# Optimization experiments

Hardware: AMD Instinct MI355X
Metric: run time of the kernel (lower is better)

## Reference

```python
import jax, jax.numpy as jnp
import numpy as np

N, T, H = 4000, 32, 64      # N = batch_size*n_neurons, t_repetition, gcn_d
E = 1024000
NT = N * T                   # graph nodes after temporal unrolling
N_NEURONS = 500
B = N // N_NEURONS
T_EBD = 16                   # tau * t_repetition = 0.5*32
N_STEPS = 12


def setup_inputs() -> dict:
    key = jax.random.key(0)
    ks = jax.random.split(key, 13)
    s = 1.0 / np.sqrt(H)
    return {
        "node_features": jax.random.normal(ks[0], (N, T, H), jnp.float32),
        "edge_index_batch": jax.random.randint(ks[1], (2, E), 0, NT, jnp.int32),
        "edge_attr_batch": jax.random.uniform(ks[2], (E,), jnp.float32),
        "batch": jax.random.randint(ks[3], (N,), 0, B, jnp.int32),
        # GRU params (1 layer, torch layout: W_ih [3H,H], W_hh [3H,H])
        "gru_Wih": jax.random.normal(ks[4], (3 * H, H), jnp.float32) * s,
        "gru_Whh": jax.random.normal(ks[5], (3 * H, H), jnp.float32) * s,
        "gru_bih": jax.random.normal(ks[6], (3 * H,), jnp.float32) * s,
        "gru_bhh": jax.random.normal(ks[7], (3 * H,), jnp.float32) * s,
        # GCNConv linear weight [out,in], no bias
        "gcn_W": jax.random.normal(ks[8], (H, H), jnp.float32) * s,
        # temporal attention MLP: Linear(T->T_ebd), Linear(T_ebd->T), no bias
        "attn_W1": jax.random.normal(ks[9], (T_EBD, T), jnp.float32) * (1.0 / np.sqrt(T)),
        "attn_W2": jax.random.normal(ks[10], (T, T_EBD), jnp.float32) * (1.0 / np.sqrt(T_EBD)),
        # final head Linear(gcn_d -> n_steps) with bias
        "fc_W": jax.random.normal(ks[11], (N_STEPS, H), jnp.float32) * s,
        "fc_b": jax.random.normal(ks[12], (N_STEPS,), jnp.float32) * s,
    }


def _gru(x, Wih, Whh, bih, bhh):
    # x: [N, T, H] -> outputs [N, T, H] (torch GRU equations, h0 = 0)
    xg = x @ Wih.T + bih  # [N, T, 3H], input projection precomputed

    def step(h, xg_t):
        hg = h @ Whh.T + bhh
        xr, xz, xn = jnp.split(xg_t, 3, axis=-1)
        hr, hz, hn = jnp.split(hg, 3, axis=-1)
        r = jax.nn.sigmoid(xr + hr)
        z = jax.nn.sigmoid(xz + hz)
        n = jnp.tanh(xn + r * hn)
        h_new = (1.0 - z) * n + z * h
        return h_new, h_new

    h0 = jnp.zeros((x.shape[0], Whh.shape[1]), x.dtype)
    _, hs = jax.lax.scan(step, h0, jnp.swapaxes(xg, 0, 1))  # hs: [T, N, H]
    return jnp.swapaxes(hs, 0, 1)


def _gcn(x, W, edge_index, edge_weight, n_nodes):
    # PyG GCNConv: add self-loops (weight 1), symmetric deg^-1/2 norm, no bias
    loops = jnp.arange(n_nodes, dtype=edge_index.dtype)
    src = jnp.concatenate([edge_index[0], loops])
    dst = jnp.concatenate([edge_index[1], loops])
    w = jnp.concatenate([edge_weight, jnp.ones((n_nodes,), edge_weight.dtype)])
    xw = x @ W.T                                            # [NT, H]
    deg = jax.ops.segment_sum(w, dst, num_segments=n_nodes)
    dis = jnp.where(deg > 0, jax.lax.rsqrt(jnp.where(deg > 0, deg, 1.0)), 0.0)
    norm = dis[src] * w * dis[dst]                          # [E+NT]
    msgs = norm[:, None] * xw[src]                          # gather + scale
    return jax.ops.segment_sum(msgs, dst, num_segments=n_nodes)


def reference(node_features, edge_index_batch, edge_attr_batch, batch,
              gru_Wih, gru_Whh, gru_bih, gru_bhh, gcn_W,
              attn_W1, attn_W2, fc_W, fc_b):
    # DGRLayer: GRU over time, then GCN over the flattened (node,time) graph
    g = _gru(node_features, gru_Wih, gru_Whh, gru_bih, gru_bhh)  # [N, T, H]
    x = g.reshape(NT, H)
    x = _gcn(x, gcn_W, edge_index_batch, edge_attr_batch, NT)
    x3 = x.reshape(N, T, H)

    # TemporalAttention (reshape mirrors torch contiguous .view semantics)
    xt = x3.reshape(B, T, N_NEURONS * H).mean(axis=-1)           # [B, T]
    attn = jax.nn.sigmoid(jax.nn.relu(xt @ attn_W1.T) @ attn_W2.T)  # [B, T]

    nf = x3.reshape(B, T, N_NEURONS, H)
    pooled = jnp.sum(attn[:, :, None, None] * nf, axis=(1, 2))   # [B, H]
    return pooled @ fc_W.T + fc_b                                # [B, n_steps]
```

## Files before the change

kernel.cpp:

```cpp
#include <hip/hip_runtime.h>
#include <hip/hip_fp16.h>

#define NNODES   4000
#define TSTEPS   32
#define HDIM     64
#define ECOUNT   1024000
#define NTOT     128000
#define BATCHB   8
#define NNEUR    500
#define TEBD     16
#define NSTEPS   12

#define CNT_SHIFT 23
#define SUM_MASK  0x7FFFFFu
#define SUM_SCALE 262144.0f
#define SLOTS     32
#define REC_BLOCKS  (NNODES / 16)
#define HIST_BLOCKS (ECOUNT / 256)
#define SCALE_BLOCKS (NTOT * HDIM / 8 / 256)

#define ROWS_PER_WAVE  5
#define ROWS_PER_BLOCK 20
#define GATHER_BLOCKS  (NTOT / ROWS_PER_BLOCK)

typedef _Float16 half8_t __attribute__((ext_vector_type(8)));
typedef float    f32x4_t __attribute__((ext_vector_type(4)));

__device__ __forceinline__ float sigmoidf_(float x) {
    return 1.0f / (1.0f + __expf(-x));
}
__device__ __forceinline__ float tanhf_(float x) {
    return 1.0f - 2.0f / (1.0f + __expf(2.0f * x));
}

__global__ __launch_bounds__(256) void k_recHist(
    const float* __restrict__ x, const float* __restrict__ Wih,
    const float* __restrict__ Whh, const float* __restrict__ bih,
    const float* __restrict__ bhh, const float* __restrict__ Wg,
    _Float16* __restrict__ xwh,
    const int* __restrict__ ei, const float* __restrict__ ea,
    unsigned* __restrict__ dc, unsigned* __restrict__ se32)
{
    __shared__ __align__(16) _Float16 hbuf[2][16 * 72];

    const int tid = threadIdx.x;

    if (blockIdx.x >= REC_BLOCKS) {
        int e = (blockIdx.x - REC_BLOCKS) * 256 + tid;
        int s = ei[e], d = ei[ECOUNT + e];
        float w = ea[e];
        unsigned q = (unsigned)(w * 32768.0f + 0.5f); q = q > 32767u ? 32767u : q;
        unsigned fx = (unsigned)(w * SUM_SCALE + 0.5f);
        unsigned old = atomicAdd(&dc[d], (1u << CNT_SHIFT) | fx);
        int r = (int)(old >> CNT_SHIFT);
        if (r < SLOTS)
            se32[d * SLOTS + r] = ((unsigned)s << 15) | q;
        return;
    }

    const int lane = tid & 63;
    const int wv   = tid >> 6;
    const int c    = lane & 15;
    const int quad = lane >> 4;
    const int n0   = blockIdx.x * 16;

    auto makeB = [&](const float* W, int row, int k0) -> half8_t {
        const float4* p = (const float4*)(W + (size_t)row * HDIM + k0);
        float4 u = p[0], v = p[1];
        half8_t h;
        h[0] = (_Float16)u.x; h[1] = (_Float16)u.y; h[2] = (_Float16)u.z; h[3] = (_Float16)u.w;
        h[4] = (_Float16)v.x; h[5] = (_Float16)v.y; h[6] = (_Float16)v.z; h[7] = (_Float16)v.w;
        return h;
    };

    half8_t Bxr[2], Bxz[2], Bxn[2], Bhr[2], Bhz[2], Bhn[2], Bw[2];
#pragma unroll
    for (int kt = 0; kt < 2; ++kt) {
        int k0 = kt * 32 + quad * 8;
        Bxr[kt] = makeB(Wih, wv * 16 + c, k0);
        Bxz[kt] = makeB(Wih, 64 + wv * 16 + c, k0);
        Bxn[kt] = makeB(Wih, 128 + wv * 16 + c, k0);
        Bhr[kt] = makeB(Whh, wv * 16 + c, k0);
        Bhz[kt] = makeB(Whh, 64 + wv * 16 + c, k0);
        Bhn[kt] = makeB(Whh, 128 + wv * 16 + c, k0);
        Bw[kt]  = makeB(Wg, wv * 16 + c, k0);
    }

    const int f = wv * 16 + c;
    const float brz_r = bih[f] + bhh[f];
    const float brz_z = bih[64 + f] + bhh[64 + f];
    const float bin_  = bih[128 + f];
    const float bhn_  = bhh[128 + f];

    float hreg[4] = {0.f, 0.f, 0.f, 0.f};
    half8_t ah[2];

    const float* xp = x + (size_t)(n0 + c) * (TSTEPS * HDIM) + quad * 8;

    float4 xq0[4], xq1[4];
    {
        const float* p0 = xp;
        xq0[0] = *(const float4*)(p0);      xq0[1] = *(const float4*)(p0 + 4);
        xq0[2] = *(const float4*)(p0 + 32); xq0[3] = *(const float4*)(p0 + 36);
        const float* p1 = xp + HDIM;
        xq1[0] = *(const float4*)(p1);      xq1[1] = *(const float4*)(p1 + 4);
        xq1[2] = *(const float4*)(p1 + 32); xq1[3] = *(const float4*)(p1 + 36);
    }

    auto step = [&](int t, float4* xq) {
        half8_t ax[2];
#pragma unroll
        for (int kt = 0; kt < 2; ++kt) {
            float4 u = xq[kt * 2], v = xq[kt * 2 + 1];
            half8_t a;
            a[0] = (_Float16)u.x; a[1] = (_Float16)u.y; a[2] = (_Float16)u.z; a[3] = (_Float16)u.w;
            a[4] = (_Float16)v.x; a[5] = (_Float16)v.y; a[6] = (_Float16)v.z; a[7] = (_Float16)v.w;
            ax[kt] = a;
        }
        if (t + 2 < TSTEPS) {
            const float* pt = xp + (size_t)(t + 2) * HDIM;
            xq[0] = *(const float4*)(pt);      xq[1] = *(const float4*)(pt + 4);
            xq[2] = *(const float4*)(pt + 32); xq[3] = *(const float4*)(pt + 36);
        }

        f32x4_t Cr  = (f32x4_t){0.f, 0.f, 0.f, 0.f};
        f32x4_t Cz  = (f32x4_t){0.f, 0.f, 0.f, 0.f};
        f32x4_t Cnx = (f32x4_t){0.f, 0.f, 0.f, 0.f};
        f32x4_t Cnh = (f32x4_t){0.f, 0.f, 0.f, 0.f};

#pragma unroll
        for (int kt = 0; kt < 2; ++kt) {
            Cr  = __builtin_amdgcn_mfma_f32_16x16x32_f16(ax[kt], Bxr[kt], Cr, 0, 0, 0);
            Cz  = __builtin_amdgcn_mfma_f32_16x16x32_f16(ax[kt], Bxz[kt], Cz, 0, 0, 0);
            Cnx = __builtin_amdgcn_mfma_f32_16x16x32_f16(ax[kt], Bxn[kt], Cnx, 0, 0, 0);
        }
        if (t > 0) {
#pragma unroll
            for (int kt = 0; kt < 2; ++kt) {
                Cr  = __builtin_amdgcn_mfma_f32_16x16x32_f16(ah[kt], Bhr[kt], Cr, 0, 0, 0);
                Cz  = __builtin_amdgcn_mfma_f32_16x16x32_f16(ah[kt], Bhz[kt], Cz, 0, 0, 0);
                Cnh = __builtin_amdgcn_mfma_f32_16x16x32_f16(ah[kt], Bhn[kt], Cnh, 0, 0, 0);
            }
        }

        _Float16* hb = hbuf[t & 1];
#pragma unroll
        for (int r = 0; r < 4; ++r) {
            float rr = sigmoidf_(Cr[r] + brz_r);
            float zz = sigmoidf_(Cz[r] + brz_z);
            float nn = tanhf_(Cnx[r] + bin_ + rr * (Cnh[r] + bhn_));
            float hn = (1.0f - zz) * nn + zz * hreg[r];
            hreg[r] = hn;
            hb[(quad * 4 + r) * 72 + f] = (_Float16)hn;
        }

        __syncthreads();

#pragma unroll
        for (int kt = 0; kt < 2; ++kt)
            ah[kt] = *(half8_t*)&hb[c * 72 + kt * 32 + quad * 8];

        f32x4_t Cw = (f32x4_t){0.f, 0.f, 0.f, 0.f};
#pragma unroll
        for (int kt = 0; kt < 2; ++kt)
            Cw = __builtin_amdgcn_mfma_f32_16x16x32_f16(ah[kt], Bw[kt], Cw, 0, 0, 0);

#pragma unroll
        for (int r = 0; r < 4; ++r) {
            int row = (n0 + quad * 4 + r) * TSTEPS + t;
            xwh[(size_t)row * HDIM + f] = (_Float16)Cw[r];
        }
    };

#pragma unroll 1
    for (int tt = 0; tt < TSTEPS; tt += 2) {
        step(tt, xq0);
        step(tt + 1, xq1);
    }
}

__global__ __launch_bounds__(256) void k_scale(
    _Float16* __restrict__ xwh, const unsigned* __restrict__ dc)
{
    const int t = blockIdx.x * 256 + threadIdx.x;
    const int row = t >> 3;
    const float dd = rsqrtf(1.0f + (float)(dc[row] & SUM_MASK) * 0x1p-18f);
    half8_t v = *(half8_t*)&xwh[(size_t)t * 8];
#pragma unroll
    for (int i = 0; i < 8; ++i) v[i] = (_Float16)((float)v[i] * dd);
    *(half8_t*)&xwh[(size_t)t * 8] = v;
}

__global__ __launch_bounds__(256) void k_gather(
    const _Float16* __restrict__ xws, const unsigned* __restrict__ dc,
    const unsigned* __restrict__ se32, float* __restrict__ S)
{
    const int tid  = threadIdx.x;
    const int lane = tid & 63;
    const int wv   = tid >> 6;
    const int d0   = blockIdx.x * ROWS_PER_BLOCK + wv * ROWS_PER_WAVE;

    unsigned pk[ROWS_PER_WAVE];
    float    sf[ROWS_PER_WAVE];
#pragma unroll
    for (int i = 0; i < ROWS_PER_WAVE; ++i) pk[i] = dc[d0 + i];
#pragma unroll
    for (int i = 0; i < ROWS_PER_WAVE; ++i)
        sf[i] = (float)xws[(size_t)(d0 + i) * HDIM + lane];

    float acc = 0.f;
#pragma unroll
    for (int i = 0; i < ROWS_PER_WAVE; ++i) {
        const int d = d0 + i;
        const float dd = rsqrtf(1.0f + (float)(pk[i] & SUM_MASK) * 0x1p-18f);
        int cnt = (int)(pk[i] >> CNT_SHIFT);
        cnt = cnt < SLOTS ? cnt : SLOTS;
        const unsigned* bkt = se32 + (size_t)d * SLOTS;

        float a0 = sf[i];
        float a1 = 0.f, a2 = 0.f, a3 = 0.f;
        int j = 0;
        for (; j + 8 <= cnt; j += 8) {
            uint4 qa = *(const uint4*)(bkt + j);
            uint4 qb = *(const uint4*)(bkt + j + 4);
            float v0 = (float)xws[(size_t)(qa.x >> 15) * HDIM + lane];
            float v1 = (float)xws[(size_t)(qa.y >> 15) * HDIM + lane];
            float v2 = (float)xws[(size_t)(qa.z >> 15) * HDIM + lane];
            float v3 = (float)xws[(size_t)(qa.w >> 15) * HDIM + lane];
            float v4 = (float)xws[(size_t)(qb.x >> 15) * HDIM + lane];
            float v5 = (float)xws[(size_t)(qb.y >> 15) * HDIM + lane];
            float v6 = (float)xws[(size_t)(qb.z >> 15) * HDIM + lane];
            float v7 = (float)xws[(size_t)(qb.w >> 15) * HDIM + lane];
            a0 = fmaf((float)(qa.x & 0x7FFFu) * 0x1p-15f, v0, a0);
            a1 = fmaf((float)(qa.y & 0x7FFFu) * 0x1p-15f, v1, a1);
            a2 = fmaf((float)(qa.z & 0x7FFFu) * 0x1p-15f, v2, a2);
            a3 = fmaf((float)(qa.w & 0x7FFFu) * 0x1p-15f, v3, a3);
            a0 = fmaf((float)(qb.x & 0x7FFFu) * 0x1p-15f, v4, a0);
            a1 = fmaf((float)(qb.y & 0x7FFFu) * 0x1p-15f, v5, a1);
            a2 = fmaf((float)(qb.z & 0x7FFFu) * 0x1p-15f, v6, a2);
            a3 = fmaf((float)(qb.w & 0x7FFFu) * 0x1p-15f, v7, a3);
        }
        for (; j + 4 <= cnt; j += 4) {
            uint4 q = *(const uint4*)(bkt + j);
            float v0 = (float)xws[(size_t)(q.x >> 15) * HDIM + lane];
            float v1 = (float)xws[(size_t)(q.y >> 15) * HDIM + lane];
            float v2 = (float)xws[(size_t)(q.z >> 15) * HDIM + lane];
            float v3 = (float)xws[(size_t)(q.w >> 15) * HDIM + lane];
            a0 = fmaf((float)(q.x & 0x7FFFu) * 0x1p-15f, v0, a0);
            a1 = fmaf((float)(q.y & 0x7FFFu) * 0x1p-15f, v1, a1);
            a2 = fmaf((float)(q.z & 0x7FFFu) * 0x1p-15f, v2, a2);
            a3 = fmaf((float)(q.w & 0x7FFFu) * 0x1p-15f, v3, a3);
        }
        for (; j < cnt; ++j) {
            unsigned u = bkt[j];
            a0 = fmaf((float)(u & 0x7FFFu) * 0x1p-15f,
                      (float)xws[(size_t)(u >> 15) * HDIM + lane], a0);
        }
        acc = fmaf(dd, (a0 + a1) + (a2 + a3), acc);
    }

    __shared__ float red[256];
    red[tid] = acc;
    __syncthreads();
    if (tid < 64) {
        float s = red[tid] + red[64 + tid] + red[128 + tid] + red[192 + tid];
        atomicAdd(&S[((blockIdx.x * ROWS_PER_BLOCK) / NNEUR) * HDIM + tid], s);
    }
}

__global__ __launch_bounds__(256) void k_final(
    const float* __restrict__ S, const float* __restrict__ W1,
    const float* __restrict__ W2, const float* __restrict__ fcW,
    const float* __restrict__ fcb, float* __restrict__ out)
{
    __shared__ float xt[256];
    __shared__ float a1[128];
    __shared__ float attn[256];
    __shared__ float pooled[512];
    const int tid = threadIdx.x;

    {
        float s = 0.f;
        const float* p = S + tid * 64;
#pragma unroll
        for (int hh = 0; hh < 64; ++hh) s += p[hh];
        xt[tid] = s * (1.0f / 32000.0f);
    }
    __syncthreads();
    if (tid < 128) {
        int b = tid >> 4, i = tid & 15;
        float s = 0.f;
#pragma unroll
        for (int t = 0; t < 32; ++t) s += xt[b * 32 + t] * W1[i * 32 + t];
        a1[tid] = fmaxf(s, 0.f);
    }
    __syncthreads();
    {
        int b = tid >> 5, t = tid & 31;
        float s = 0.f;
#pragma unroll
        for (int i = 0; i < 16; ++i) s += a1[b * 16 + i] * W2[t * 16 + i];
        attn[tid] = 1.0f / (1.0f + __expf(-s));
    }
    __syncthreads();
    for (int o = tid; o < 512; o += 256) {
        int b = o >> 6, h = o & 63;
        float s = 0.f;
#pragma unroll
        for (int t = 0; t < 32; ++t) s += attn[b * 32 + t] * S[(b * 32 + t) * 64 + h];
        pooled[o] = s;
    }
    __syncthreads();
    if (tid < BATCHB * NSTEPS) {
        int b = tid / NSTEPS, st = tid % NSTEPS;
        float acc = fcb[st];
#pragma unroll
        for (int h = 0; h < 64; ++h) acc += pooled[b * 64 + h] * fcW[st * 64 + h];
        out[b * NSTEPS + st] = acc;
    }
}

extern "C" void kernel_launch(void* const* d_in, const int* in_sizes, int n_in,
                              void* d_out, int out_size, void* d_ws, size_t ws_size,
                              hipStream_t stream) {
    const float* x   = (const float*)d_in[0];
    const int*   ei  = (const int*)  d_in[1];
    const float* ea  = (const float*)d_in[2];
    const float* Wih = (const float*)d_in[4];
    const float* Whh = (const float*)d_in[5];
    const float* bih = (const float*)d_in[6];
    const float* bhh = (const float*)d_in[7];
    const float* Wg  = (const float*)d_in[8];
    const float* W1  = (const float*)d_in[9];
    const float* W2  = (const float*)d_in[10];
    const float* fcW = (const float*)d_in[11];
    const float* fcb = (const float*)d_in[12];
    float* out = (float*)d_out;

    char* p = (char*)d_ws;
    unsigned* dc = (unsigned*)p;   p += sizeof(unsigned) * NTOT;
    float* S = (float*)p;          p += sizeof(float) * 256 * HDIM;
    unsigned* se32 = (unsigned*)p; p += sizeof(unsigned) * (size_t)NTOT * SLOTS;
    _Float16* xwh = (_Float16*)p;  p += sizeof(_Float16) * (size_t)NTOT * HDIM;

    hipMemsetAsync(dc, 0, sizeof(unsigned) * NTOT + sizeof(float) * 256 * HDIM, stream);
    k_recHist <<<REC_BLOCKS + HIST_BLOCKS, 256, 0, stream>>>(
        x, Wih, Whh, bih, bhh, Wg, xwh, ei, ea, dc, se32);
    k_scale   <<<SCALE_BLOCKS, 256, 0, stream>>>(xwh, dc);
    k_gather  <<<GATHER_BLOCKS, 256, 0, stream>>>(xwh, dc, se32, S);
    k_final   <<<1, 256, 0, stream>>>(S, W1, W2, fcW, fcb, out);
}
```

Before: 228.9 us.

## Replace per-destination edge gather with dense source-by-group aggregation matrix GEMM

Only per-(batch,time) group sums of the GCN output are needed downstream. The change therefore accumulates normalized edge weights into a dense 16-bit fixed-point matrix indexed by source node and destination group, then multiplies it against the scaled features in a blocked fp16 multiply-accumulate kernel. Partial results are merged per group, together with self-loops. This removes the slot-based per-destination gather of feature rows, at the cost of zeroing and streaming a large matrix of about 65 MB. It also brings fixed-point packed atomics and fp16 accumulation that may lose precision or overflow. The old path is kept as a fallback when the workspace is too small.

```diff
diff --git a/kernel.cpp b/kernel.cpp
--- a/kernel.cpp
+++ b/kernel.cpp
@@ -11,19 +11,30 @@
 #define TEBD     16
 #define NSTEPS   12
 
+#define REC_BLOCKS  (NNODES / 16)
+
+#define HISTF_BLOCKS (ECOUNT / 256)
+#define ZERO_BLOCKS  2000
+#define NBT          256
+#define MBYTES       ((size_t)NTOT * NBT * 2)
+#define MB_BLOCKS    (ECOUNT / 256)
+#define SCALE_BLOCKS (NTOT * HDIM / 8 / 256)
+#define GEMM_BLOCKS  256
+#define CHUNK_SRC    (NTOT / GEMM_BLOCKS)
+#define PPART        (NBT * HDIM)
+#define MAIN_WS      (512000 + 65536 + 65536000 + 16777216 + 16384000)
+
 #define CNT_SHIFT 23
 #define SUM_MASK  0x7FFFFFu
 #define SUM_SCALE 262144.0f
 #define SLOTS     32
-#define REC_BLOCKS  (NNODES / 16)
 #define HIST_BLOCKS (ECOUNT / 256)
-#define SCALE_BLOCKS (NTOT * HDIM / 8 / 256)
-
 #define ROWS_PER_WAVE  5
 #define ROWS_PER_BLOCK 20
 #define GATHER_BLOCKS  (NTOT / ROWS_PER_BLOCK)
 
 typedef _Float16 half8_t __attribute__((ext_vector_type(8)));
+typedef _Float16 half2_t __attribute__((ext_vector_type(2)));
 typedef float    f32x4_t __attribute__((ext_vector_type(4)));
 
 __device__ __forceinline__ float sigmoidf_(float x) {
@@ -31,6 +42,253 @@
 }
 __device__ __forceinline__ float tanhf_(float x) {
     return 1.0f - 2.0f / (1.0f + __expf(2.0f * x));
+}
+
+__device__ __forceinline__ void gru_body(
+    const float* __restrict__ x, const float* __restrict__ Wih,
+    const float* __restrict__ Whh, const float* __restrict__ bih,
+    const float* __restrict__ bhh, const float* __restrict__ Wg,
+    _Float16* __restrict__ xwh, _Float16 (*hbuf)[16 * 72], int tid, int blk)
+{
+    const int lane = tid & 63;
+    const int wv   = tid >> 6;
+    const int c    = lane & 15;
+    const int quad = lane >> 4;
+    const int n0   = blk * 16;
+
+    auto makeB = [&](const float* W, int row, int k0) -> half8_t {
+        const float4* p = (const float4*)(W + (size_t)row * HDIM + k0);
+        float4 u = p[0], v = p[1];
+        half8_t h;
+        h[0] = (_Float16)u.x; h[1] = (_Float16)u.y; h[2] = (_Float16)u.z; h[3] = (_Float16)u.w;
+        h[4] = (_Float16)v.x; h[5] = (_Float16)v.y; h[6] = (_Float16)v.z; h[7] = (_Float16)v.w;
+        return h;
+    };
+
+    half8_t Bxr[2], Bxz[2], Bxn[2], Bhr[2], Bhz[2], Bhn[2], Bw[2];
+#pragma unroll
+    for (int kt = 0; kt < 2; ++kt) {
+        int k0 = kt * 32 + quad * 8;
+        Bxr[kt] = makeB(Wih, wv * 16 + c, k0);
+        Bxz[kt] = makeB(Wih, 64 + wv * 16 + c, k0);
+        Bxn[kt] = makeB(Wih, 128 + wv * 16 + c, k0);
+        Bhr[kt] = makeB(Whh, wv * 16 + c, k0);
+        Bhz[kt] = makeB(Whh, 64 + wv * 16 + c, k0);
+        Bhn[kt] = makeB(Whh, 128 + wv * 16 + c, k0);
+        Bw[kt]  = makeB(Wg, wv * 16 + c, k0);
+    }
+
+    const int f = wv * 16 + c;
+    const float brz_r = bih[f] + bhh[f];
+    const float brz_z = bih[64 + f] + bhh[64 + f];
+    const float bin_  = bih[128 + f];
+    const float bhn_  = bhh[128 + f];
+
+    float hreg[4] = {0.f, 0.f, 0.f, 0.f};
+    half8_t ah[2];
+
+    const float* xp = x + (size_t)(n0 + c) * (TSTEPS * HDIM) + quad * 8;
+
+    float4 xq0[4], xq1[4];
+    {
+        const float* p0 = xp;
+        xq0[0] = *(const float4*)(p0);      xq0[1] = *(const float4*)(p0 + 4);
+        xq0[2] = *(const float4*)(p0 + 32); xq0[3] = *(const float4*)(p0 + 36);
+        const float* p1 = xp + HDIM;
+        xq1[0] = *(const float4*)(p1);      xq1[1] = *(const float4*)(p1 + 4);
+        xq1[2] = *(const float4*)(p1 + 32); xq1[3] = *(const float4*)(p1 + 36);
+    }
+
+    auto step = [&](int t, float4* xq) {
+        half8_t ax[2];
+#pragma unroll
+        for (int kt = 0; kt < 2; ++kt) {
+            float4 u = xq[kt * 2], v = xq[kt * 2 + 1];
+            half8_t a;
+            a[0] = (_Float16)u.x; a[1] = (_Float16)u.y; a[2] = (_Float16)u.z; a[3] = (_Float16)u.w;
+            a[4] = (_Float16)v.x; a[5] = (_Float16)v.y; a[6] = (_Float16)v.z; a[7] = (_Float16)v.w;
+            ax[kt] = a;
+        }
+        if (t + 2 < TSTEPS) {
+            const float* pt = xp + (size_t)(t + 2) * HDIM;
+            xq[0] = *(const float4*)(pt);      xq[1] = *(const float4*)(pt + 4);
+            xq[2] = *(const float4*)(pt + 32); xq[3] = *(const float4*)(pt + 36);
+        }
+
+        f32x4_t Cr  = (f32x4_t){0.f, 0.f, 0.f, 0.f};
+        f32x4_t Cz  = (f32x4_t){0.f, 0.f, 0.f, 0.f};
+        f32x4_t Cnx = (f32x4_t){0.f, 0.f, 0.f, 0.f};
+        f32x4_t Cnh = (f32x4_t){0.f, 0.f, 0.f, 0.f};
+
+#pragma unroll
+        for (int kt = 0; kt < 2; ++kt) {
+            Cr  = __builtin_amdgcn_mfma_f32_16x16x32_f16(ax[kt], Bxr[kt], Cr, 0, 0, 0);
+            Cz  = __builtin_amdgcn_mfma_f32_16x16x32_f16(ax[kt], Bxz[kt], Cz, 0, 0, 0);
+            Cnx = __builtin_amdgcn_mfma_f32_16x16x32_f16(ax[kt], Bxn[kt], Cnx, 0, 0, 0);
+        }
+        if (t > 0) {
+#pragma unroll
+            for (int kt = 0; kt < 2; ++kt) {
+                Cr  = __builtin_amdgcn_mfma_f32_16x16x32_f16(ah[kt], Bhr[kt], Cr, 0, 0, 0);
+                Cz  = __builtin_amdgcn_mfma_f32_16x16x32_f16(ah[kt], Bhz[kt], Cz, 0, 0, 0);
+                Cnh = __builtin_amdgcn_mfma_f32_16x16x32_f16(ah[kt], Bhn[kt], Cnh, 0, 0, 0);
+            }
+        }
+
+        _Float16* hb = hbuf[t & 1];
+#pragma unroll
+        for (int r = 0; r < 4; ++r) {
+            float rr = sigmoidf_(Cr[r] + brz_r);
+            float zz = sigmoidf_(Cz[r] + brz_z);
+            float nn = tanhf_(Cnx[r] + bin_ + rr * (Cnh[r] + bhn_));
+            float hn = (1.0f - zz) * nn + zz * hreg[r];
+            hreg[r] = hn;
+            hb[(quad * 4 + r) * 72 + f] = (_Float16)hn;
+        }
+
+        __syncthreads();
+
+#pragma unroll
+        for (int kt = 0; kt < 2; ++kt)
+            ah[kt] = *(half8_t*)&hb[c * 72 + kt * 32 + quad * 8];
+
+        f32x4_t Cw = (f32x4_t){0.f, 0.f, 0.f, 0.f};
+#pragma unroll
+        for (int kt = 0; kt < 2; ++kt)
+            Cw = __builtin_amdgcn_mfma_f32_16x16x32_f16(ah[kt], Bw[kt], Cw, 0, 0, 0);
+
+#pragma unroll
+        for (int r = 0; r < 4; ++r) {
+            int row = (n0 + quad * 4 + r) * TSTEPS + t;
+            xwh[(size_t)row * HDIM + f] = (_Float16)Cw[r];
+        }
+    };
+
+#pragma unroll 1
+    for (int tt = 0; tt < TSTEPS; tt += 2) {
+        step(tt, xq0);
+        step(tt + 1, xq1);
+    }
+}
+
+
+__global__ __launch_bounds__(256) void k_recHZ(
+    const float* __restrict__ x, const float* __restrict__ Wih,
+    const float* __restrict__ Whh, const float* __restrict__ bih,
+    const float* __restrict__ bhh, const float* __restrict__ Wg,
+    _Float16* __restrict__ xwh,
+    const int* __restrict__ ei, const float* __restrict__ ea,
+    float* __restrict__ dw, uint4* __restrict__ Mz)
+{
+    __shared__ __align__(16) _Float16 hbuf[2][16 * 72];
+    const int tid = threadIdx.x;
+
+    if (blockIdx.x >= REC_BLOCKS + HISTF_BLOCKS) {
+        const int zb = blockIdx.x - (REC_BLOCKS + HISTF_BLOCKS);
+        uint4* p = Mz + (size_t)zb * 2048;
+        uint4 z; z.x = 0; z.y = 0; z.z = 0; z.w = 0;
+#pragma unroll
+        for (int i = 0; i < 8; ++i) p[i * 256 + tid] = z;
+        return;
+    }
+    if (blockIdx.x >= REC_BLOCKS) {
+        int e = (blockIdx.x - REC_BLOCKS) * 256 + tid;
+        atomicAdd(&dw[ei[ECOUNT + e]], ea[e]);
+        return;
+    }
+    gru_body(x, Wih, Whh, bih, bhh, Wg, xwh, hbuf, tid, blockIdx.x);
+}
+
+__global__ __launch_bounds__(256) void k_scaleF(
+    _Float16* __restrict__ xwh, const float* __restrict__ dw)
+{
+    const int t = blockIdx.x * 256 + threadIdx.x;
+    const int row = t >> 3;
+    const float dd = rsqrtf(1.0f + dw[row]);
+    half8_t v = *(half8_t*)&xwh[(size_t)t * 8];
+#pragma unroll
+    for (int i = 0; i < 8; ++i) v[i] = (_Float16)((float)v[i] * dd);
+    *(half8_t*)&xwh[(size_t)t * 8] = v;
+}
+
+__global__ __launch_bounds__(256) void k_Mbuild(
+    const int* __restrict__ ei, const float* __restrict__ ea,
+    const float* __restrict__ dw, unsigned* __restrict__ M32)
+{
+    int e = blockIdx.x * 256 + threadIdx.x;
+    int s = ei[e], d = ei[ECOUNT + e];
+    float c = ea[e] * rsqrtf(1.0f + dw[d]);
+    unsigned bt = (unsigned)d / 500u;
+    unsigned fx = (unsigned)(c * 4096.0f + 0.5f);
+    unsigned val = (bt & 1u) ? (fx << 16) : fx;
+    atomicAdd(&M32[(size_t)s * 128 + (bt >> 1)], val);
+}
+
+__global__ __launch_bounds__(512) void k_gemm(
+    const _Float16* __restrict__ xws, const unsigned short* __restrict__ Mu,
+    float* __restrict__ Ppart)
+{
+    const int tid = threadIdx.x;
+    const int bt  = tid & 255;
+    const int hh  = tid >> 8;
+    const int base = blockIdx.x * CHUNK_SRC;
+
+    half2_t acc2[16];
+#pragma unroll
+    for (int j = 0; j < 16; ++j) acc2[j] = (half2_t){(_Float16)0.f, (_Float16)0.f};
+
+#pragma unroll 1
+    for (int b = 0; b < CHUNK_SRC; b += 4) {
+#pragma unroll
+        for (int u = 0; u < 4; ++u) {
+            const int sidx = base + b + u;
+            unsigned short cell = Mu[(size_t)sidx * NBT + bt];
+            _Float16 mh = (_Float16)((float)cell * 0x1p-12f);
+            half2_t m2 = (half2_t){mh, mh};
+            const half2_t* xr = (const half2_t*)&xws[(size_t)sidx * HDIM + hh * 32];
+#pragma unroll
+            for (int j = 0; j < 16; ++j)
+                acc2[j] += m2 * xr[j];
+        }
+    }
+
+    float* dst = Ppart + (size_t)blockIdx.x * PPART + bt * HDIM + hh * 32;
+#pragma unroll
+    for (int j = 0; j < 16; j += 2) {
+        f32x4_t f;
+        f[0] = (float)acc2[j][0];     f[1] = (float)acc2[j][1];
+        f[2] = (float)acc2[j + 1][0]; f[3] = (float)acc2[j + 1][1];
+        *(f32x4_t*)&dst[j * 2] = f;
+    }
+}
+
+__global__ __launch_bounds__(256) void k_mergeM(
+    const float* __restrict__ Ppart, const _Float16* __restrict__ xws,
+    const float* __restrict__ dw, float* __restrict__ S)
+{
+    const int bt  = blockIdx.x;
+    const int tid = threadIdx.x;
+    const int h   = tid & 63;
+    const int q   = tid >> 6;
+
+    float s = 0.f;
+    const float* bp = Ppart + (size_t)bt * HDIM + h;
+#pragma unroll 4
+    for (int c = q * 64; c < q * 64 + 64; ++c)
+        s += bp[(size_t)c * PPART];
+
+    const int dbase = bt * NNEUR + q * 125;
+#pragma unroll 1
+    for (int r = 0; r < 125; ++r) {
+        int d = dbase + r;
+        s += rsqrtf(1.0f + dw[d]) * (float)xws[(size_t)d * HDIM + h];
+    }
+
+    __shared__ float red[256];
+    red[tid] = s;
+    __syncthreads();
+    if (tid < 64)
+        S[bt * 64 + tid] = red[tid] + red[64 + tid] + red[128 + tid] + red[192 + tid];
 }
 
 __global__ __launch_bounds__(256) void k_recHist(
@@ -42,7 +300,6 @@
     unsigned* __restrict__ dc, unsigned* __restrict__ se32)
 {
     __shared__ __align__(16) _Float16 hbuf[2][16 * 72];
-
     const int tid = threadIdx.x;
 
     if (blockIdx.x >= REC_BLOCKS) {
@@ -57,126 +314,7 @@
             se32[d * SLOTS + r] = ((unsigned)s << 15) | q;
         return;
     }
-
-    const int lane = tid & 63;
-    const int wv   = tid >> 6;
-    const int c    = lane & 15;
-    const int quad = lane >> 4;
-    const int n0   = blockIdx.x * 16;
-
-    auto makeB = [&](const float* W, int row, int k0) -> half8_t {
-        const float4* p = (const float4*)(W + (size_t)row * HDIM + k0);
-        float4 u = p[0], v = p[1];
-        half8_t h;
-        h[0] = (_Float16)u.x; h[1] = (_Float16)u.y; h[2] = (_Float16)u.z; h[3] = (_Float16)u.w;
-        h[4] = (_Float16)v.x; h[5] = (_Float16)v.y; h[6] = (_Float16)v.z; h[7] = (_Float16)v.w;
-        return h;
-    };
-
-    half8_t Bxr[2], Bxz[2], Bxn[2], Bhr[2], Bhz[2], Bhn[2], Bw[2];
-#pragma unroll
-    for (int kt = 0; kt < 2; ++kt) {
-        int k0 = kt * 32 + quad * 8;
-        Bxr[kt] = makeB(Wih, wv * 16 + c, k0);
-        Bxz[kt] = makeB(Wih, 64 + wv * 16 + c, k0);
-        Bxn[kt] = makeB(Wih, 128 + wv * 16 + c, k0);
-        Bhr[kt] = makeB(Whh, wv * 16 + c, k0);
-        Bhz[kt] = makeB(Whh, 64 + wv * 16 + c, k0);
-        Bhn[kt] = makeB(Whh, 128 + wv * 16 + c, k0);
-        Bw[kt]  = makeB(Wg, wv * 16 + c, k0);
-    }
-
-    const int f = wv * 16 + c;
-    const float brz_r = bih[f] + bhh[f];
-    const float brz_z = bih[64 + f] + bhh[64 + f];
-    const float bin_  = bih[128 + f];
-    const float bhn_  = bhh[128 + f];
-
-    float hreg[4] = {0.f, 0.f, 0.f, 0.f};
-    half8_t ah[2];
-
-    const float* xp = x + (size_t)(n0 + c) * (TSTEPS * HDIM) + quad * 8;
-
-    float4 xq0[4], xq1[4];
-    {
-        const float* p0 = xp;
-        xq0[0] = *(const float4*)(p0);      xq0[1] = *(const float4*)(p0 + 4);
-        xq0[2] = *(const float4*)(p0 + 32); xq0[3] = *(const float4*)(p0 + 36);
-        const float* p1 = xp + HDIM;
-        xq1[0] = *(const float4*)(p1);      xq1[1] = *(const float4*)(p1 + 4);
-        xq1[2] = *(const float4*)(p1 + 32); xq1[3] = *(const float4*)(p1 + 36);
-    }
-
-    auto step = [&](int t, float4* xq) {
-        half8_t ax[2];
-#pragma unroll
-        for (int kt = 0; kt < 2; ++kt) {
-            float4 u = xq[kt * 2], v = xq[kt * 2 + 1];
-            half8_t a;
-            a[0] = (_Float16)u.x; a[1] = (_Float16)u.y; a[2] = (_Float16)u.z; a[3] = (_Float16)u.w;
-            a[4] = (_Float16)v.x; a[5] = (_Float16)v.y; a[6] = (_Float16)v.z; a[7] = (_Float16)v.w;
-            ax[kt] = a;
-        }
-        if (t + 2 < TSTEPS) {
-            const float* pt = xp + (size_t)(t + 2) * HDIM;
-            xq[0] = *(const float4*)(pt);      xq[1] = *(const float4*)(pt + 4);
-            xq[2] = *(const float4*)(pt + 32); xq[3] = *(const float4*)(pt + 36);
-        }
-
-        f32x4_t Cr  = (f32x4_t){0.f, 0.f, 0.f, 0.f};
-        f32x4_t Cz  = (f32x4_t){0.f, 0.f, 0.f, 0.f};
-        f32x4_t Cnx = (f32x4_t){0.f, 0.f, 0.f, 0.f};
-        f32x4_t Cnh = (f32x4_t){0.f, 0.f, 0.f, 0.f};
-
-#pragma unroll
-        for (int kt = 0; kt < 2; ++kt) {
-            Cr  = __builtin_amdgcn_mfma_f32_16x16x32_f16(ax[kt], Bxr[kt], Cr, 0, 0, 0);
-            Cz  = __builtin_amdgcn_mfma_f32_16x16x32_f16(ax[kt], Bxz[kt], Cz, 0, 0, 0);
-            Cnx = __builtin_amdgcn_mfma_f32_16x16x32_f16(ax[kt], Bxn[kt], Cnx, 0, 0, 0);
-        }
-        if (t > 0) {
-#pragma unroll
-            for (int kt = 0; kt < 2; ++kt) {
-                Cr  = __builtin_amdgcn_mfma_f32_16x16x32_f16(ah[kt], Bhr[kt], Cr, 0, 0, 0);
-                Cz  = __builtin_amdgcn_mfma_f32_16x16x32_f16(ah[kt], Bhz[kt], Cz, 0, 0, 0);
-                Cnh = __builtin_amdgcn_mfma_f32_16x16x32_f16(ah[kt], Bhn[kt], Cnh, 0, 0, 0);
-            }
-        }
-
-        _Float16* hb = hbuf[t & 1];
-#pragma unroll
-        for (int r = 0; r < 4; ++r) {
-            float rr = sigmoidf_(Cr[r] + brz_r);
-            float zz = sigmoidf_(Cz[r] + brz_z);
-            float nn = tanhf_(Cnx[r] + bin_ + rr * (Cnh[r] + bhn_));
-            float hn = (1.0f - zz) * nn + zz * hreg[r];
-            hreg[r] = hn;
-            hb[(quad * 4 + r) * 72 + f] = (_Float16)hn;
-        }
-
-        __syncthreads();
-
-#pragma unroll
-        for (int kt = 0; kt < 2; ++kt)
-            ah[kt] = *(half8_t*)&hb[c * 72 + kt * 32 + quad * 8];
-
-        f32x4_t Cw = (f32x4_t){0.f, 0.f, 0.f, 0.f};
-#pragma unroll
-        for (int kt = 0; kt < 2; ++kt)
-            Cw = __builtin_amdgcn_mfma_f32_16x16x32_f16(ah[kt], Bw[kt], Cw, 0, 0, 0);
-
-#pragma unroll
-        for (int r = 0; r < 4; ++r) {
-            int row = (n0 + quad * 4 + r) * TSTEPS + t;
-            xwh[(size_t)row * HDIM + f] = (_Float16)Cw[r];
-        }
-    };
-
-#pragma unroll 1
-    for (int tt = 0; tt < TSTEPS; tt += 2) {
-        step(tt, xq0);
-        step(tt + 1, xq1);
-    }
+    gru_body(x, Wih, Whh, bih, bhh, Wg, xwh, hbuf, tid, blockIdx.x);
 }
 
 __global__ __launch_bounds__(256) void k_scale(
@@ -337,16 +475,34 @@
     const float* fcb = (const float*)d_in[12];
     float* out = (float*)d_out;
 
-    char* p = (char*)d_ws;
-    unsigned* dc = (unsigned*)p;   p += sizeof(unsigned) * NTOT;
-    float* S = (float*)p;          p += sizeof(float) * 256 * HDIM;
-    unsigned* se32 = (unsigned*)p; p += sizeof(unsigned) * (size_t)NTOT * SLOTS;
-    _Float16* xwh = (_Float16*)p;  p += sizeof(_Float16) * (size_t)NTOT * HDIM;
-
-    hipMemsetAsync(dc, 0, sizeof(unsigned) * NTOT + sizeof(float) * 256 * HDIM, stream);
-    k_recHist <<<REC_BLOCKS + HIST_BLOCKS, 256, 0, stream>>>(
-        x, Wih, Whh, bih, bhh, Wg, xwh, ei, ea, dc, se32);
-    k_scale   <<<SCALE_BLOCKS, 256, 0, stream>>>(xwh, dc);
-    k_gather  <<<GATHER_BLOCKS, 256, 0, stream>>>(xwh, dc, se32, S);
-    k_final   <<<1, 256, 0, stream>>>(S, W1, W2, fcW, fcb, out);
-}
+    if (ws_size >= (size_t)MAIN_WS) {
+        char* p = (char*)d_ws;
+        float* dw = (float*)p;         p += 512000;
+        float* S  = (float*)p;         p += 65536;
+        char*  M  = p;                 p += MBYTES;
+        float* Ppart = (float*)p;      p += sizeof(float) * GEMM_BLOCKS * PPART;
+        _Float16* xwh = (_Float16*)p;
+
+        (void)hipMemsetAsync(dw, 0, 512000, stream);
+        k_recHZ  <<<REC_BLOCKS + HISTF_BLOCKS + ZERO_BLOCKS, 256, 0, stream>>>(
+            x, Wih, Whh, bih, bhh, Wg, xwh, ei, ea, dw, (uint4*)M);
+        k_scaleF <<<SCALE_BLOCKS, 256, 0, stream>>>(xwh, dw);
+        k_Mbuild <<<MB_BLOCKS, 256, 0, stream>>>(ei, ea, dw, (unsigned*)M);
+        k_gemm   <<<GEMM_BLOCKS, 512, 0, stream>>>(xwh, (const unsigned short*)M, Ppart);
+        k_mergeM <<<NBT, 256, 0, stream>>>(Ppart, xwh, dw, S);
+        k_final  <<<1, 256, 0, stream>>>(S, W1, W2, fcW, fcb, out);
+    } else {
+        char* p = (char*)d_ws;
+        unsigned* dc = (unsigned*)p;   p += sizeof(unsigned) * NTOT;
+        float* S = (float*)p;          p += sizeof(float) * 256 * HDIM;
+        unsigned* se32 = (unsigned*)p; p += sizeof(unsigned) * (size_t)NTOT * SLOTS;
+        _Float16* xwh = (_Float16*)p;
+
+        (void)hipMemsetAsync(dc, 0, sizeof(unsigned) * NTOT + sizeof(float) * 256 * HDIM, stream);
+        k_recHist <<<REC_BLOCKS + HIST_BLOCKS, 256, 0, stream>>>(
+            x, Wih, Whh, bih, bhh, Wg, xwh, ei, ea, dc, se32);
+        k_scale   <<<SCALE_BLOCKS, 256, 0, stream>>>(xwh, dc);
+        k_gather  <<<GATHER_BLOCKS, 256, 0, stream>>>(xwh, dc, se32, S);
+        k_final   <<<1, 256, 0, stream>>>(S, W1, W2, fcW, fcb, out);
+    }
+}
```

Measured after the change: 412.3 us. +80.2%, slower.
